# Optimization experiments

Measured on AMD Instinct MI355X. Metric: run time of the kernel, lower is better.

## Reference

```python
import jax, jax.numpy as jnp
import numpy as np

N, E, DIM, EDIM, H, T = 30000, 300000, 64, 16, 3, 6


def setup_inputs() -> dict:
    key = jax.random.key(0)
    ks = jax.random.split(key, 20)
    s = 0.1
    inp = {
        'x': jax.random.normal(ks[0], (N, DIM), jnp.float32),
        'edge_index': jax.random.randint(ks[1], (2, E), 0, N, jnp.int64),
        'edge_attr': jax.random.normal(ks[2], (E, EDIM), jnp.float32),
        # EdgeGATConv params (heads=3, out per head = DIM, concat=False -> head mean)
        'Wg': jax.random.normal(ks[3], (DIM, H * DIM), jnp.float32) * s,
        'bg': jnp.zeros((DIM,), jnp.float32),
        'a_src': jax.random.normal(ks[4], (H, DIM), jnp.float32) * s,
        'a_dst': jax.random.normal(ks[5], (H, DIM), jnp.float32) * s,
        'We': jax.random.normal(ks[6], (EDIM, H * DIM), jnp.float32) * s,
        'a_edge': jax.random.normal(ks[7], (H, DIM), jnp.float32) * s,
        # GRU (1 layer), torch gate order: r, z, n
        'Wih': jax.random.normal(ks[8], (3 * DIM, DIM), jnp.float32) * s,
        'Whh': jax.random.normal(ks[9], (3 * DIM, DIM), jnp.float32) * s,
        'bih': jnp.zeros((3 * DIM,), jnp.float32),
        'bhh': jnp.zeros((3 * DIM,), jnp.float32),
        # NodeLevelBatchNorm per time step
        'gamma': jnp.ones((T, DIM), jnp.float32),
        'beta': jnp.zeros((T, DIM), jnp.float32),
        # final linear: dim*(T+1) -> dim
        'Wlin': jax.random.normal(ks[10], (DIM * (T + 1), DIM), jnp.float32) * s,
        'blin': jnp.zeros((DIM,), jnp.float32),
    }
    return inp


def _edge_gat(x, edge_index, edge_attr, Wg, bg, a_src, a_dst, We, a_edge):
    n = x.shape[0]
    xw = (x @ Wg).reshape(n, H, DIM)                 # [N,H,C]
    ew = (edge_attr @ We).reshape(-1, H, DIM)        # [E,H,C]
    src, dst = edge_index[0], edge_index[1]
    logits = ((xw[src] * a_src).sum(-1)
              + (xw[dst] * a_dst).sum(-1)
              + (ew * a_edge).sum(-1))               # [E,H]
    logits = jax.nn.leaky_relu(logits, 0.2)
    # segment softmax over incoming edges per destination node
    amax = jax.ops.segment_max(logits, dst, num_segments=n)
    amax = jnp.where(jnp.isfinite(amax), amax, 0.0)
    ex = jnp.exp(logits - amax[dst])
    denom = jax.ops.segment_sum(ex, dst, num_segments=n)
    att = ex / (denom[dst] + 1e-16)                  # [E,H]
    agg = jax.ops.segment_sum(xw[src] * att[..., None], dst, num_segments=n)  # [N,H,C]
    return agg.mean(axis=1) + bg                     # concat=False: head mean


def _gru_step(m, h, Wih, Whh, bih, bhh):
    gi = m @ Wih.T + bih
    gh = h @ Whh.T + bhh
    ir, iz, inn = jnp.split(gi, 3, axis=-1)
    hr, hz, hn = jnp.split(gh, 3, axis=-1)
    r = jax.nn.sigmoid(ir + hr)
    z = jax.nn.sigmoid(iz + hz)
    nn_ = jnp.tanh(inn + r * hn)
    return (1.0 - z) * nn_ + z * h


def _node_bn(x, gamma, beta, eps=1e-5):
    mu = x.mean(axis=0)
    var = ((x - mu) ** 2).mean(axis=0)
    return (x - mu) * jax.lax.rsqrt(var + eps) * gamma + beta


def reference(x, edge_index, edge_attr, Wg, bg, a_src, a_dst, We, a_edge,
              Wih, Whh, bih, bhh, gamma, beta, Wlin, blin):
    h = x
    feats = [x]
    for i in range(T):
        m = jax.nn.celu(_edge_gat(x, edge_index, edge_attr, Wg, bg, a_src, a_dst, We, a_edge))
        h = _gru_step(m, h, Wih, Whh, bih, bhh)
        x = _node_bn(h, gamma[i], beta[i])
        feats.append(x)
    return jnp.concatenate(feats, axis=-1) @ Wlin + blin
```

## Files before the change

kernel.cpp:

```cpp
#include <hip/hip_runtime.h>
#include <math.h>

constexpr int N_ = 30000;
constexpr int E_ = 300000;
constexpr int SCB = (N_ + 255) / 256;

using f32x4  = __attribute__((ext_vector_type(4))) float;
using bf16x8 = __attribute__((ext_vector_type(8))) short;

__device__ __forceinline__ float4 ldg4(const float* p){ return *reinterpret_cast<const float4*>(p); }

__device__ __forceinline__ unsigned short f2bf(float f){
  union { float f; unsigned int u; } v; v.f = f;
  unsigned int r = v.u + 0x7FFFu + ((v.u >> 16) & 1u);
  return (unsigned short)(r >> 16);
}
__device__ __forceinline__ float bf2f(unsigned short b){
  union { unsigned int u; float f; } v; v.u = ((unsigned int)b) << 16;
  return v.f;
}
__device__ __forceinline__ float sigmoidf_(float x){ return 1.0f/(1.0f + __expf(-x)); }


__global__ void k_zero(int* __restrict__ deg){
  int i = blockIdx.x*256 + threadIdx.x;
  if (i < N_) deg[i] = 0;
}

__global__ void k_wfrag(const float* __restrict__ Wg, const float* __restrict__ Wih,
                        const float* __restrict__ Whh, const float* __restrict__ Wlin,
                        const float* __restrict__ We, const float* __restrict__ a_edge,
                        unsigned short* __restrict__ fG, unsigned short* __restrict__ fI,
                        unsigned short* __restrict__ fH, unsigned short* __restrict__ fL,
                        float* __restrict__ P){
  if (blockIdx.x == 256){
    int t = threadIdx.x; if (t >= 48) return;
    int j = t / 3, h = t % 3;
    float s = 0.f;
    for (int c = 0; c < 64; ++c) s += We[j*192 + h*64 + c] * a_edge[h*64 + c];
    P[j*3 + h] = s;
    return;
  }
  int id = blockIdx.x*256 + threadIdx.x;
  int lid, KT;
  unsigned short* dst; int mode;
  if (id < 12288)      { lid = id;         KT = 2;  dst = fG; mode = 0; }
  else if (id < 24576) { lid = id - 12288; KT = 2;  dst = fI; mode = 1; }
  else if (id < 36864) { lid = id - 24576; KT = 2;  dst = fH; mode = 2; }
  else                 { lid = id - 36864; KT = 14; dst = fL; mode = 3; }
  int j = lid & 7, l = (lid >> 3) & 63, rest = lid >> 9;
  int kt = rest % KT, nt = rest / KT;
  int k = kt*32 + (l>>4)*8 + j;
  int n = nt*16 + (l&15);
  float v;
  if (mode == 0)      v = Wg[k*192 + n];
  else if (mode == 1) v = Wih[n*64 + k];
  else if (mode == 2) v = Whh[n*64 + k];
  else                v = Wlin[k*64 + n];
  dst[lid] = f2bf(v);
}

__global__ void k_hist(const int* __restrict__ ei, int* __restrict__ deg){
  int e = blockIdx.x*256 + threadIdx.x;
  if (e < E_) atomicAdd(&deg[ei[E_ + e]], 1);
}

__global__ void k_scanA(const int* __restrict__ deg, int* __restrict__ partial){
  int i = blockIdx.x*256 + threadIdx.x;
  int v = (i < N_) ? deg[i] : 0;
  #pragma unroll
  for (int off = 1; off < 64; off <<= 1) v += __shfl_xor(v, off);
  __shared__ int ws[4];
  if ((threadIdx.x & 63) == 0) ws[threadIdx.x >> 6] = v;
  __syncthreads();
  if (threadIdx.x == 0) partial[blockIdx.x] = ws[0] + ws[1] + ws[2] + ws[3];
}

__global__ void k_scanB(int* __restrict__ partial, int* __restrict__ row_ptr){
  __shared__ int s[128];
  int t = threadIdx.x;
  int v = (t < SCB) ? partial[t] : 0;
  s[t] = v; __syncthreads();
  for (int off = 1; off < 128; off <<= 1){
    int u = (t >= off) ? s[t-off] : 0;
    __syncthreads();
    s[t] += u;
    __syncthreads();
  }
  if (t < SCB) partial[t] = s[t] - v;
  if (t == 0) row_ptr[N_] = E_;
}

__global__ void k_scanC(const int* __restrict__ deg, const int* __restrict__ partial,
                        int* __restrict__ row_ptr, int* __restrict__ cursor){
  __shared__ int s[256];
  int t = threadIdx.x, i = blockIdx.x*256 + t;
  int v = (i < N_) ? deg[i] : 0;
  s[t] = v; __syncthreads();
  for (int off = 1; off < 256; off <<= 1){
    int u = (t >= off) ? s[t-off] : 0;
    __syncthreads();
    s[t] += u;
    __syncthreads();
  }
  int ex = s[t] - v + partial[blockIdx.x];
  if (i < N_){ row_ptr[i] = ex; cursor[i] = ex; }
}

__global__ void k_scatter(const int* __restrict__ ei, const float* __restrict__ edge_attr,
                          const float* __restrict__ P,
                          int* __restrict__ cursor, int* __restrict__ src_s,
                          int* __restrict__ dst_s, float* __restrict__ el_s){
  __shared__ float sP[48];
  int t = threadIdx.x;
  if (t < 48) sP[t] = P[t];
  __syncthreads();
  int e = blockIdx.x*256 + t;
  if (e >= E_) return;
  const float* ea = edge_attr + (size_t)e*16;
  float v[16];
  #pragma unroll
  for (int q = 0; q < 4; ++q){
    float4 f = ldg4(ea + q*4);
    v[q*4+0]=f.x; v[q*4+1]=f.y; v[q*4+2]=f.z; v[q*4+3]=f.w;
  }
  float l0=0.f,l1=0.f,l2=0.f;
  #pragma unroll
  for (int j = 0; j < 16; ++j){
    l0 += v[j]*sP[j*3+0]; l1 += v[j]*sP[j*3+1]; l2 += v[j]*sP[j*3+2];
  }
  int d = ei[E_ + e];
  int p = atomicAdd(&cursor[d], 1);
  src_s[p] = ei[e];
  dst_s[p] = d;
  el_s[p*3+0] = l0; el_s[p*3+1] = l1; el_s[p*3+2] = l2;
}


__global__ __launch_bounds__(256) void k_xw(
    const float* __restrict__ hsrc,
    const float* __restrict__ bn_stats,
    const float* __restrict__ gamma, const float* __restrict__ beta,
    int gidx, int bn, int slot,
    const unsigned short* __restrict__ fG,
    const float* __restrict__ a_src, const float* __restrict__ a_dst,
    unsigned short* __restrict__ xw,
    float* __restrict__ asrc, float* __restrict__ adst,
    float* __restrict__ feats)
{
  __shared__ short sAf[8*64*8];
  __shared__ unsigned short sXW[64*196];
  __shared__ float sSc[64], sSh[64];
  const int t = threadIdx.x;
  const int row0 = blockIdx.x * 64;
  if (t < 64){
    float sc = 1.f, sh = 0.f;
    if (bn){
      float mu  = bn_stats[t] * (1.0f/30000.0f);
      float var = bn_stats[64+t] * (1.0f/30000.0f) - mu*mu;
      float rs = rsqrtf(var + 1e-5f);
      sc = gamma[gidx*64 + t] * rs;
      sh = beta[gidx*64 + t] - mu*sc;
    }
    sSc[t] = sc; sSh[t] = sh;
  }
  __syncthreads();
  {
    const int lr = t >> 4, k4 = (t & 15) * 4;
    const float sc0=sSc[k4],sc1=sSc[k4+1],sc2=sSc[k4+2],sc3=sSc[k4+3];
    const float sh0=sSh[k4],sh1=sSh[k4+1],sh2=sSh[k4+2],sh3=sSh[k4+3];
    const int kt = k4 >> 5, lanew = lr + (((k4>>3)&3)<<4), j0 = k4 & 7;
    #pragma unroll
    for (int i = 0; i < 4; ++i){
      int r = lr + i*16, gr = row0 + r;
      float4 v = make_float4(0.f,0.f,0.f,0.f);
      if (gr < N_){
        v = ldg4(hsrc + (size_t)gr*64 + k4);
        v.x = fmaf(v.x, sc0, sh0); v.y = fmaf(v.y, sc1, sh1);
        v.z = fmaf(v.z, sc2, sh2); v.w = fmaf(v.w, sc3, sh3);
        *reinterpret_cast<float4*>(feats + (size_t)gr*448 + slot*64 + k4) = v;
      }
      ushort4 pk; pk.x=f2bf(v.x); pk.y=f2bf(v.y); pk.z=f2bf(v.z); pk.w=f2bf(v.w);
      *reinterpret_cast<ushort4*>(&sAf[((i*2+kt)*64 + lanew)*8 + j0]) = pk;
    }
  }
  __syncthreads();
  const int w = t >> 6, l = t & 63, q = l >> 4, b = l & 15;
  f32x4 acc[12];
  #pragma unroll
  for (int nt = 0; nt < 12; ++nt) acc[nt] = (f32x4){0.f,0.f,0.f,0.f};
  bf16x8 a0 = *reinterpret_cast<bf16x8*>(&sAf[((w*2+0)*64 + l)*8]);
  bf16x8 a1 = *reinterpret_cast<bf16x8*>(&sAf[((w*2+1)*64 + l)*8]);
  #pragma unroll
  for (int nt = 0; nt < 12; ++nt){
    bf16x8 b0 = *reinterpret_cast<const bf16x8*>(fG + (size_t)((nt*2+0)*64 + l)*8);
    bf16x8 b1 = *reinterpret_cast<const bf16x8*>(fG + (size_t)((nt*2+1)*64 + l)*8);
    acc[nt] = __builtin_amdgcn_mfma_f32_16x16x32_bf16(a0, b0, acc[nt], 0, 0, 0);
    acc[nt] = __builtin_amdgcn_mfma_f32_16x16x32_bf16(a1, b1, acc[nt], 0, 0, 0);
  }
  float asl[3][4], adl[3][4];
  #pragma unroll
  for (int h = 0; h < 3; ++h)
    #pragma unroll
    for (int u = 0; u < 4; ++u){
      asl[h][u] = a_src[h*64 + u*16 + b];
      adl[h][u] = a_dst[h*64 + u*16 + b];
    }
  #pragma unroll
  for (int r = 0; r < 4; ++r){
    int gr = row0 + w*16 + q*4 + r;
    #pragma unroll
    for (int h = 0; h < 3; ++h){
      float s = 0.f, d = 0.f;
      #pragma unroll
      for (int u = 0; u < 4; ++u){
        s = fmaf(acc[4*h+u][r], asl[h][u], s);
        d = fmaf(acc[4*h+u][r], adl[h][u], d);
      }
      s += __shfl_xor(s,1); s += __shfl_xor(s,2); s += __shfl_xor(s,4); s += __shfl_xor(s,8);
      d += __shfl_xor(d,1); d += __shfl_xor(d,2); d += __shfl_xor(d,4); d += __shfl_xor(d,8);
      if (b == h && gr < N_){ asrc[gr*3+h] = s; adst[gr*3+h] = d; }
    }
  }
  #pragma unroll
  for (int nt = 0; nt < 12; ++nt){
    int col = nt*16 + b;
    #pragma unroll
    for (int r = 0; r < 4; ++r)
      sXW[(w*16 + q*4 + r)*196 + col] = f2bf(acc[nt][r]);
  }
  __syncthreads();
  #pragma unroll
  for (int i = 0; i < 12; ++i){
    int id = i*256 + t;
    int row = id / 48, cg = id % 48, gr = row0 + row;
    if (gr < N_){
      ushort4 pv = *reinterpret_cast<ushort4*>(&sXW[row*196 + cg*4]);
      *reinterpret_cast<ushort4*>(xw + (size_t)gr*192 + cg*4) = pv;
    }
  }
}

__global__ void k_att(const int* __restrict__ src_s, const int* __restrict__ dst_s,
                      const float* __restrict__ el_s,
                      const float* __restrict__ asrc, const float* __restrict__ adst,
                      float* __restrict__ att_s){
  int p = blockIdx.x*256 + threadIdx.x;
  if (p >= E_) return;
  int s = src_s[p], d = dst_s[p];
  #pragma unroll
  for (int h = 0; h < 3; ++h){
    float l = asrc[s*3+h] + adst[d*3+h] + el_s[p*3+h];
    l = l > 0.f ? l : 0.2f*l;
    att_s[p*3+h] = __expf(l);
  }
}

__global__ __launch_bounds__(256) void k_agg(
    const int* __restrict__ row_ptr, const int* __restrict__ src_s,
    const float* __restrict__ att_s,
    const unsigned short* __restrict__ xw,
    const float* __restrict__ bg,
    float* __restrict__ mbuf, float* __restrict__ bn_stats)
{
  if (blockIdx.x == 0 && threadIdx.x < 128) bn_stats[threadIdx.x] = 0.f;
  int n = blockIdx.x*4 + (threadIdx.x >> 6);
  int c = threadIdx.x & 63;
  if (n >= N_) return;
  int p0 = row_ptr[n], p1 = row_ptr[n+1];
  float d0 = 0.f, d1 = 0.f, d2 = 0.f;
  float a0 = 0.f, a1 = 0.f, a2 = 0.f;
  int p = p0;
  for (; p + 2 <= p1; p += 2){
    int sA = src_s[p], sB = src_s[p+1];
    float wA0 = att_s[p*3+0], wA1 = att_s[p*3+1], wA2 = att_s[p*3+2];
    float wB0 = att_s[p*3+3], wB1 = att_s[p*3+4], wB2 = att_s[p*3+5];
    const unsigned short* xpA = xw + (size_t)sA*192 + c;
    const unsigned short* xpB = xw + (size_t)sB*192 + c;
    float vA0 = bf2f(xpA[0]), vA1 = bf2f(xpA[64]), vA2 = bf2f(xpA[128]);
    float vB0 = bf2f(xpB[0]), vB1 = bf2f(xpB[64]), vB2 = bf2f(xpB[128]);
    d0 += wA0 + wB0; d1 += wA1 + wB1; d2 += wA2 + wB2;
    a0 = fmaf(wA0, vA0, a0); a1 = fmaf(wA1, vA1, a1); a2 = fmaf(wA2, vA2, a2);
    a0 = fmaf(wB0, vB0, a0); a1 = fmaf(wB1, vB1, a1); a2 = fmaf(wB2, vB2, a2);
  }
  if (p < p1){
    int s = src_s[p];
    float w0 = att_s[p*3+0], w1 = att_s[p*3+1], w2 = att_s[p*3+2];
    const unsigned short* xp = xw + (size_t)s*192 + c;
    d0 += w0; d1 += w1; d2 += w2;
    a0 = fmaf(w0, bf2f(xp[0]), a0);
    a1 = fmaf(w1, bf2f(xp[64]), a1);
    a2 = fmaf(w2, bf2f(xp[128]), a2);
  }
  float mp = (a0/(d0+1e-16f) + a1/(d1+1e-16f) + a2/(d2+1e-16f)) * (1.0f/3.0f) + bg[c];
  mbuf[(size_t)n*64 + c] = mp > 0.f ? mp : (__expf(mp) - 1.0f);
}

__global__ __launch_bounds__(256) void k_gru(
    const float* __restrict__ mbuf, const float* __restrict__ hsrc,
    float* __restrict__ hbuf,
    const unsigned short* __restrict__ fI, const unsigned short* __restrict__ fH,
    const float* __restrict__ bih, const float* __restrict__ bhh,
    float* __restrict__ bn_stats)
{
  __shared__ short sMf[8*64*8];
  __shared__ short sHf[8*64*8];
  __shared__ float sH[64][68];
  __shared__ float sStat[128];
  const int t = threadIdx.x;
  const int row0 = blockIdx.x * 64;
  if (t < 128) sStat[t] = 0.f;
  {
    const int lr = t >> 4, k4 = (t & 15) * 4;
    const int kt = k4 >> 5, lanew = lr + (((k4>>3)&3)<<4), j0 = k4 & 7;
    #pragma unroll
    for (int i = 0; i < 4; ++i){
      int r = lr + i*16, gr = row0 + r;
      float4 vm = make_float4(0.f,0.f,0.f,0.f), vh = vm;
      if (gr < N_){ vm = ldg4(mbuf + (size_t)gr*64 + k4); vh = ldg4(hsrc + (size_t)gr*64 + k4); }
      ushort4 pm; pm.x=f2bf(vm.x); pm.y=f2bf(vm.y); pm.z=f2bf(vm.z); pm.w=f2bf(vm.w);
      ushort4 ph; ph.x=f2bf(vh.x); ph.y=f2bf(vh.y); ph.z=f2bf(vh.z); ph.w=f2bf(vh.w);
      *reinterpret_cast<ushort4*>(&sMf[((i*2+kt)*64 + lanew)*8 + j0]) = pm;
      *reinterpret_cast<ushort4*>(&sHf[((i*2+kt)*64 + lanew)*8 + j0]) = ph;
      sH[r][k4+0]=vh.x; sH[r][k4+1]=vh.y; sH[r][k4+2]=vh.z; sH[r][k4+3]=vh.w;
    }
  }
  __syncthreads();
  const int w = t >> 6, l = t & 63, q = l >> 4, b = l & 15;
  f32x4 aI[12], aH[12];
  #pragma unroll
  for (int nt = 0; nt < 12; ++nt){ aI[nt] = (f32x4){0.f,0.f,0.f,0.f}; aH[nt] = (f32x4){0.f,0.f,0.f,0.f}; }
  bf16x8 am0 = *reinterpret_cast<bf16x8*>(&sMf[((w*2+0)*64 + l)*8]);
  bf16x8 am1 = *reinterpret_cast<bf16x8*>(&sMf[((w*2+1)*64 + l)*8]);
  bf16x8 ah0 = *reinterpret_cast<bf16x8*>(&sHf[((w*2+0)*64 + l)*8]);
  bf16x8 ah1 = *reinterpret_cast<bf16x8*>(&sHf[((w*2+1)*64 + l)*8]);
  #pragma unroll
  for (int nt = 0; nt < 12; ++nt){
    bf16x8 bI0 = *reinterpret_cast<const bf16x8*>(fI + (size_t)((nt*2+0)*64 + l)*8);
    bf16x8 bI1 = *reinterpret_cast<const bf16x8*>(fI + (size_t)((nt*2+1)*64 + l)*8);
    bf16x8 bH0 = *reinterpret_cast<const bf16x8*>(fH + (size_t)((nt*2+0)*64 + l)*8);
    bf16x8 bH1 = *reinterpret_cast<const bf16x8*>(fH + (size_t)((nt*2+1)*64 + l)*8);
    aI[nt] = __builtin_amdgcn_mfma_f32_16x16x32_bf16(am0, bI0, aI[nt], 0, 0, 0);
    aI[nt] = __builtin_amdgcn_mfma_f32_16x16x32_bf16(am1, bI1, aI[nt], 0, 0, 0);
    aH[nt] = __builtin_amdgcn_mfma_f32_16x16x32_bf16(ah0, bH0, aH[nt], 0, 0, 0);
    aH[nt] = __builtin_amdgcn_mfma_f32_16x16x32_bf16(ah1, bH1, aH[nt], 0, 0, 0);
  }
  float s1[4] = {0.f,0.f,0.f,0.f}, s2[4] = {0.f,0.f,0.f,0.f};
  #pragma unroll
  for (int tt = 0; tt < 4; ++tt){
    int c = tt*16 + b;
    float bir = bih[c], biz = bih[64+c], bin = bih[128+c];
    float bhr = bhh[c], bhz = bhh[64+c], bhn = bhh[128+c];
    #pragma unroll
    for (int r = 0; r < 4; ++r){
      int row = w*16 + q*4 + r, gr = row0 + row;
      float rg = sigmoidf_(aI[tt][r]   + bir + aH[tt][r]   + bhr);
      float zg = sigmoidf_(aI[tt+4][r] + biz + aH[tt+4][r] + bhz);
      float ng = tanhf(aI[tt+8][r] + bin + rg*(aH[tt+8][r] + bhn));
      float ho = sH[row][c];
      float hv = (1.f - zg)*ng + zg*ho;
      if (gr < N_){
        hbuf[(size_t)gr*64 + c] = hv;
        s1[tt] += hv; s2[tt] += hv*hv;
      }
    }
  }
  #pragma unroll
  for (int tt = 0; tt < 4; ++tt){
    float v = s1[tt];
    v += __shfl_xor(v, 16); v += __shfl_xor(v, 32);
    float u = s2[tt];
    u += __shfl_xor(u, 16); u += __shfl_xor(u, 32);
    if (q == 0){
      atomicAdd(&sStat[tt*16 + b], v);
      atomicAdd(&sStat[64 + tt*16 + b], u);
    }
  }
  __syncthreads();
  if (t < 128) atomicAdd(&bn_stats[t], sStat[t]);
}

__global__ __launch_bounds__(256) void k_final(
    const float* __restrict__ feats, const float* __restrict__ hbuf,
    const float* __restrict__ bn_stats,
    const float* __restrict__ gamma, const float* __restrict__ beta,
    const unsigned short* __restrict__ fL, const float* __restrict__ blin,
    float* __restrict__ out)
{
  __shared__ short sAf[8*64*8];
  __shared__ float sSc[64], sSh[64];
  const int t = threadIdx.x;
  const int row0 = blockIdx.x * 64;
  if (t < 64){
    float mu  = bn_stats[t] * (1.0f/30000.0f);
    float var = bn_stats[64+t] * (1.0f/30000.0f) - mu*mu;
    float rs = rsqrtf(var + 1e-5f);
    float sc = gamma[5*64 + t] * rs;
    sSc[t] = sc;
    sSh[t] = beta[5*64 + t] - mu*sc;
  }
  const int w = t >> 6, l = t & 63, q = l >> 4, b = l & 15;
  const int lr = t >> 4, k4 = (t & 15) * 4;
  const int kt = k4 >> 5, lanew = lr + (((k4>>3)&3)<<4), j0 = k4 & 7;
  f32x4 acc[4];
  #pragma unroll
  for (int nt = 0; nt < 4; ++nt) acc[nt] = (f32x4){0.f,0.f,0.f,0.f};
  for (int kc = 0; kc < 7; ++kc){
    __syncthreads();
    {
      #pragma unroll
      for (int i = 0; i < 4; ++i){
        int r = lr + i*16, gr = row0 + r;
        float4 v = make_float4(0.f,0.f,0.f,0.f);
        if (gr < N_){
          if (kc < 6) v = ldg4(feats + (size_t)gr*448 + kc*64 + k4);
          else {
            v = ldg4(hbuf + (size_t)gr*64 + k4);
            v.x = fmaf(v.x, sSc[k4+0], sSh[k4+0]);
            v.y = fmaf(v.y, sSc[k4+1], sSh[k4+1]);
            v.z = fmaf(v.z, sSc[k4+2], sSh[k4+2]);
            v.w = fmaf(v.w, sSc[k4+3], sSh[k4+3]);
          }
        }
        ushort4 pk; pk.x=f2bf(v.x); pk.y=f2bf(v.y); pk.z=f2bf(v.z); pk.w=f2bf(v.w);
        *reinterpret_cast<ushort4*>(&sAf[((i*2+kt)*64 + lanew)*8 + j0]) = pk;
      }
    }
    __syncthreads();
    bf16x8 a0 = *reinterpret_cast<bf16x8*>(&sAf[((w*2+0)*64 + l)*8]);
    bf16x8 a1 = *reinterpret_cast<bf16x8*>(&sAf[((w*2+1)*64 + l)*8]);
    #pragma unroll
    for (int nt = 0; nt < 4; ++nt){
      bf16x8 b0 = *reinterpret_cast<const bf16x8*>(fL + (size_t)((nt*14 + kc*2+0)*64 + l)*8);
      bf16x8 b1 = *reinterpret_cast<const bf16x8*>(fL + (size_t)((nt*14 + kc*2+1)*64 + l)*8);
      acc[nt] = __builtin_amdgcn_mfma_f32_16x16x32_bf16(a0, b0, acc[nt], 0, 0, 0);
      acc[nt] = __builtin_amdgcn_mfma_f32_16x16x32_bf16(a1, b1, acc[nt], 0, 0, 0);
    }
  }
  #pragma unroll
  for (int nt = 0; nt < 4; ++nt){
    int col = nt*16 + b;
    float bl = blin[col];
    #pragma unroll
    for (int r = 0; r < 4; ++r){
      int gr = row0 + w*16 + q*4 + r;
      if (gr < N_) out[(size_t)gr*64 + col] = acc[nt][r] + bl;
    }
  }
}


extern "C" void kernel_launch(void* const* d_in, const int* in_sizes, int n_in,
                              void* d_out, int out_size, void* d_ws, size_t ws_size,
                              hipStream_t stream) {
  const float* x        = (const float*)d_in[0];
  const int*   ei       = (const int*)  d_in[1];
  const float* edge_attr= (const float*)d_in[2];
  const float* Wg       = (const float*)d_in[3];
  const float* bg       = (const float*)d_in[4];
  const float* a_src    = (const float*)d_in[5];
  const float* a_dst    = (const float*)d_in[6];
  const float* We       = (const float*)d_in[7];
  const float* a_edge   = (const float*)d_in[8];
  const float* Wih      = (const float*)d_in[9];
  const float* Whh      = (const float*)d_in[10];
  const float* bih      = (const float*)d_in[11];
  const float* bhh      = (const float*)d_in[12];
  const float* gamma    = (const float*)d_in[13];
  const float* beta     = (const float*)d_in[14];
  const float* Wlin     = (const float*)d_in[15];
  const float* blin     = (const float*)d_in[16];
  float* out = (float*)d_out;

  char* w = (char*)d_ws;
  auto alloc = [&](size_t bytes) -> void* {
    void* p = (void*)w;
    w += (bytes + 255) & ~(size_t)255;
    return p;
  };
  int*   row_ptr = (int*)  alloc((size_t)(N_+1)*4);
  int*   deg     = (int*)  alloc((size_t)N_*4);
  int*   cursor  = (int*)  alloc((size_t)N_*4);
  int*   partial = (int*)  alloc(128*4);
  int*   src_s   = (int*)  alloc((size_t)E_*4);
  int*   dst_s   = (int*)  alloc((size_t)E_*4);
  float* el_s    = (float*)alloc((size_t)E_*3*4);
  float* att_s   = (float*)alloc((size_t)E_*3*4);
  float* Pw      = (float*)alloc(48*4);
  unsigned short* fG = (unsigned short*)alloc(12288*2);
  unsigned short* fI = (unsigned short*)alloc(12288*2);
  unsigned short* fH = (unsigned short*)alloc(12288*2);
  unsigned short* fL = (unsigned short*)alloc(28672*2);
  unsigned short* xw = (unsigned short*)alloc((size_t)N_*192*2);
  float* asrc    = (float*)alloc((size_t)N_*3*4);
  float* adst    = (float*)alloc((size_t)N_*3*4);
  float* mbuf    = (float*)alloc((size_t)N_*64*4);
  float* hbuf    = (float*)alloc((size_t)N_*64*4);
  float* feats   = (float*)alloc((size_t)N_*448*4);
  float* bn_stats= (float*)alloc(128*4);

  const int EB = (E_ + 255)/256;
  const int GEMMB = (N_ + 63)/64;

  k_zero   <<<SCB, 256, 0, stream>>>(deg);
  k_wfrag  <<<257, 256, 0, stream>>>(Wg, Wih, Whh, Wlin, We, a_edge, fG, fI, fH, fL, Pw);
  k_hist   <<<EB, 256, 0, stream>>>(ei, deg);
  k_scanA  <<<SCB, 256, 0, stream>>>(deg, partial);
  k_scanB  <<<1, 128, 0, stream>>>(partial, row_ptr);
  k_scanC  <<<SCB, 256, 0, stream>>>(deg, partial, row_ptr, cursor);
  k_scatter<<<EB, 256, 0, stream>>>(ei, edge_attr, Pw, cursor, src_s, dst_s, el_s);

  for (int step = 0; step < 6; ++step){
    const float* hsrc = (step == 0) ? x : hbuf;
    k_xw <<<GEMMB, 256, 0, stream>>>(hsrc, bn_stats, gamma, beta,
                                     step-1, step > 0 ? 1 : 0, step,
                                     fG, a_src, a_dst, xw, asrc, adst, feats);
    k_att<<<EB, 256, 0, stream>>>(src_s, dst_s, el_s, asrc, adst, att_s);
    k_agg<<<(N_+3)/4, 256, 0, stream>>>(row_ptr, src_s, att_s, xw, bg, mbuf, bn_stats);
    k_gru<<<GEMMB, 256, 0, stream>>>(mbuf, hsrc, hbuf, fI, fH, bih, bhh, bn_stats);
  }
  k_final<<<GEMMB, 256, 0, stream>>>(feats, hbuf, bn_stats, gamma, beta, fL, blin, out);
}
```

Before: 586.8 us.

## Store per-step features as bf16 MFMA fragments and interleave xw heads

Per-step normalized node features are no longer written as fp32 into a wide feats matrix. Instead k_xw dumps its bf16 A-fragments straight to a fragment buffer, and k_final reads them directly as MFMA operands without restaging through LDS. The xw layout is changed to an interleaved [node][channel][4] bf16 format so k_agg gathers all three heads with one 8-byte load per edge, and its edge loop is unrolled by 4. The deg zeroing kernel is folded into k_wfrag to save a launch. The cost is a padded xw (256 vs 192 entries per node) and a small extra fragment write per step.

```diff
diff --git a/kernel.cpp b/kernel.cpp
--- a/kernel.cpp
+++ b/kernel.cpp
@@ -4,6 +4,7 @@
 constexpr int N_ = 30000;
 constexpr int E_ = 300000;
 constexpr int SCB = (N_ + 255) / 256;
+constexpr int GB_ = (N_ + 63) / 64;
 
 using f32x4  = __attribute__((ext_vector_type(4))) float;
 using bf16x8 = __attribute__((ext_vector_type(8))) short;
@@ -21,18 +22,18 @@
 }
 __device__ __forceinline__ float sigmoidf_(float x){ return 1.0f/(1.0f + __expf(-x)); }
 
-
-__global__ void k_zero(int* __restrict__ deg){
-  int i = blockIdx.x*256 + threadIdx.x;
-  if (i < N_) deg[i] = 0;
-}
 
 __global__ void k_wfrag(const float* __restrict__ Wg, const float* __restrict__ Wih,
                         const float* __restrict__ Whh, const float* __restrict__ Wlin,
                         const float* __restrict__ We, const float* __restrict__ a_edge,
                         unsigned short* __restrict__ fG, unsigned short* __restrict__ fI,
                         unsigned short* __restrict__ fH, unsigned short* __restrict__ fL,
-                        float* __restrict__ P){
+                        float* __restrict__ P, int* __restrict__ deg){
+  if (blockIdx.x >= 257){
+    int i = (blockIdx.x - 257)*256 + threadIdx.x;
+    if (i < N_) deg[i] = 0;
+    return;
+  }
   if (blockIdx.x == 256){
     int t = threadIdx.x; if (t >= 48) return;
     int j = t / 3, h = t % 3;
@@ -141,12 +142,12 @@
     const float* __restrict__ hsrc,
     const float* __restrict__ bn_stats,
     const float* __restrict__ gamma, const float* __restrict__ beta,
-    int gidx, int bn, int slot,
+    int gidx, int bn,
     const unsigned short* __restrict__ fG,
     const float* __restrict__ a_src, const float* __restrict__ a_dst,
     unsigned short* __restrict__ xw,
     float* __restrict__ asrc, float* __restrict__ adst,
-    float* __restrict__ feats)
+    unsigned short* __restrict__ fr)
 {
   __shared__ short sAf[8*64*8];
   __shared__ unsigned short sXW[64*196];
@@ -178,13 +179,18 @@
         v = ldg4(hsrc + (size_t)gr*64 + k4);
         v.x = fmaf(v.x, sc0, sh0); v.y = fmaf(v.y, sc1, sh1);
         v.z = fmaf(v.z, sc2, sh2); v.w = fmaf(v.w, sc3, sh3);
-        *reinterpret_cast<float4*>(feats + (size_t)gr*448 + slot*64 + k4) = v;
       }
       ushort4 pk; pk.x=f2bf(v.x); pk.y=f2bf(v.y); pk.z=f2bf(v.z); pk.w=f2bf(v.w);
       *reinterpret_cast<ushort4*>(&sAf[((i*2+kt)*64 + lanew)*8 + j0]) = pk;
     }
   }
   __syncthreads();
+  {
+    bf16x8 v0 = *reinterpret_cast<bf16x8*>(&sAf[t*8]);
+    bf16x8 v1 = *reinterpret_cast<bf16x8*>(&sAf[2048 + t*8]);
+    bf16x8* g = reinterpret_cast<bf16x8*>(fr + (size_t)blockIdx.x*4096);
+    g[t] = v0; g[256 + t] = v1;
+  }
   const int w = t >> 6, l = t & 63, q = l >> 4, b = l & 15;
   f32x4 acc[12];
   #pragma unroll
@@ -231,12 +237,16 @@
   }
   __syncthreads();
   #pragma unroll
-  for (int i = 0; i < 12; ++i){
+  for (int i = 0; i < 16; ++i){
     int id = i*256 + t;
-    int row = id / 48, cg = id % 48, gr = row0 + row;
+    int row = id >> 6, c2 = id & 63, gr = row0 + row;
     if (gr < N_){
-      ushort4 pv = *reinterpret_cast<ushort4*>(&sXW[row*196 + cg*4]);
-      *reinterpret_cast<ushort4*>(xw + (size_t)gr*192 + cg*4) = pv;
+      ushort4 pv;
+      pv.x = sXW[row*196 + c2];
+      pv.y = sXW[row*196 + 64 + c2];
+      pv.z = sXW[row*196 + 128 + c2];
+      pv.w = 0;
+      *reinterpret_cast<ushort4*>(xw + ((size_t)gr << 8) + (c2 << 2)) = pv;
     }
   }
 }
@@ -271,26 +281,32 @@
   float d0 = 0.f, d1 = 0.f, d2 = 0.f;
   float a0 = 0.f, a1 = 0.f, a2 = 0.f;
   int p = p0;
-  for (; p + 2 <= p1; p += 2){
-    int sA = src_s[p], sB = src_s[p+1];
-    float wA0 = att_s[p*3+0], wA1 = att_s[p*3+1], wA2 = att_s[p*3+2];
-    float wB0 = att_s[p*3+3], wB1 = att_s[p*3+4], wB2 = att_s[p*3+5];
-    const unsigned short* xpA = xw + (size_t)sA*192 + c;
-    const unsigned short* xpB = xw + (size_t)sB*192 + c;
-    float vA0 = bf2f(xpA[0]), vA1 = bf2f(xpA[64]), vA2 = bf2f(xpA[128]);
-    float vB0 = bf2f(xpB[0]), vB1 = bf2f(xpB[64]), vB2 = bf2f(xpB[128]);
-    d0 += wA0 + wB0; d1 += wA1 + wB1; d2 += wA2 + wB2;
-    a0 = fmaf(wA0, vA0, a0); a1 = fmaf(wA1, vA1, a1); a2 = fmaf(wA2, vA2, a2);
-    a0 = fmaf(wB0, vB0, a0); a1 = fmaf(wB1, vB1, a1); a2 = fmaf(wB2, vB2, a2);
-  }
-  if (p < p1){
+  for (; p + 4 <= p1; p += 4){
+    int sA = src_s[p], sB = src_s[p+1], sC = src_s[p+2], sD = src_s[p+3];
+    ushort4 gA = *reinterpret_cast<const ushort4*>(xw + ((size_t)sA << 8) + (c << 2));
+    ushort4 gB = *reinterpret_cast<const ushort4*>(xw + ((size_t)sB << 8) + (c << 2));
+    ushort4 gC = *reinterpret_cast<const ushort4*>(xw + ((size_t)sC << 8) + (c << 2));
+    ushort4 gD = *reinterpret_cast<const ushort4*>(xw + ((size_t)sD << 8) + (c << 2));
+    float wA0 = att_s[p*3+0],  wA1 = att_s[p*3+1],  wA2 = att_s[p*3+2];
+    float wB0 = att_s[p*3+3],  wB1 = att_s[p*3+4],  wB2 = att_s[p*3+5];
+    float wC0 = att_s[p*3+6],  wC1 = att_s[p*3+7],  wC2 = att_s[p*3+8];
+    float wD0 = att_s[p*3+9],  wD1 = att_s[p*3+10], wD2 = att_s[p*3+11];
+    d0 += (wA0 + wB0) + (wC0 + wD0);
+    d1 += (wA1 + wB1) + (wC1 + wD1);
+    d2 += (wA2 + wB2) + (wC2 + wD2);
+    a0 = fmaf(wA0, bf2f(gA.x), a0); a1 = fmaf(wA1, bf2f(gA.y), a1); a2 = fmaf(wA2, bf2f(gA.z), a2);
+    a0 = fmaf(wB0, bf2f(gB.x), a0); a1 = fmaf(wB1, bf2f(gB.y), a1); a2 = fmaf(wB2, bf2f(gB.z), a2);
+    a0 = fmaf(wC0, bf2f(gC.x), a0); a1 = fmaf(wC1, bf2f(gC.y), a1); a2 = fmaf(wC2, bf2f(gC.z), a2);
+    a0 = fmaf(wD0, bf2f(gD.x), a0); a1 = fmaf(wD1, bf2f(gD.y), a1); a2 = fmaf(wD2, bf2f(gD.z), a2);
+  }
+  for (; p < p1; ++p){
     int s = src_s[p];
+    ushort4 g = *reinterpret_cast<const ushort4*>(xw + ((size_t)s << 8) + (c << 2));
     float w0 = att_s[p*3+0], w1 = att_s[p*3+1], w2 = att_s[p*3+2];
-    const unsigned short* xp = xw + (size_t)s*192 + c;
     d0 += w0; d1 += w1; d2 += w2;
-    a0 = fmaf(w0, bf2f(xp[0]), a0);
-    a1 = fmaf(w1, bf2f(xp[64]), a1);
-    a2 = fmaf(w2, bf2f(xp[128]), a2);
+    a0 = fmaf(w0, bf2f(g.x), a0);
+    a1 = fmaf(w1, bf2f(g.y), a1);
+    a2 = fmaf(w2, bf2f(g.z), a2);
   }
   float mp = (a0/(d0+1e-16f) + a1/(d1+1e-16f) + a2/(d2+1e-16f)) * (1.0f/3.0f) + bg[c];
   mbuf[(size_t)n*64 + c] = mp > 0.f ? mp : (__expf(mp) - 1.0f);
@@ -381,7 +397,7 @@
 }
 
 __global__ __launch_bounds__(256) void k_final(
-    const float* __restrict__ feats, const float* __restrict__ hbuf,
+    const unsigned short* __restrict__ ff, const float* __restrict__ hbuf,
     const float* __restrict__ bn_stats,
     const float* __restrict__ gamma, const float* __restrict__ beta,
     const unsigned short* __restrict__ fL, const float* __restrict__ blin,
@@ -399,40 +415,51 @@
     sSc[t] = sc;
     sSh[t] = beta[5*64 + t] - mu*sc;
   }
+  __syncthreads();
   const int w = t >> 6, l = t & 63, q = l >> 4, b = l & 15;
   const int lr = t >> 4, k4 = (t & 15) * 4;
   const int kt = k4 >> 5, lanew = lr + (((k4>>3)&3)<<4), j0 = k4 & 7;
+  {
+    #pragma unroll
+    for (int i = 0; i < 4; ++i){
+      int r = lr + i*16, gr = row0 + r;
+      float4 v = make_float4(0.f,0.f,0.f,0.f);
+      if (gr < N_){
+        v = ldg4(hbuf + (size_t)gr*64 + k4);
+        v.x = fmaf(v.x, sSc[k4+0], sSh[k4+0]);
+        v.y = fmaf(v.y, sSc[k4+1], sSh[k4+1]);
+        v.z = fmaf(v.z, sSc[k4+2], sSh[k4+2]);
+        v.w = fmaf(v.w, sSc[k4+3], sSh[k4+3]);
+      }
+      ushort4 pk; pk.x=f2bf(v.x); pk.y=f2bf(v.y); pk.z=f2bf(v.z); pk.w=f2bf(v.w);
+      *reinterpret_cast<ushort4*>(&sAf[((i*2+kt)*64 + lanew)*8 + j0]) = pk;
+    }
+  }
+  __syncthreads();
   f32x4 acc[4];
   #pragma unroll
   for (int nt = 0; nt < 4; ++nt) acc[nt] = (f32x4){0.f,0.f,0.f,0.f};
-  for (int kc = 0; kc < 7; ++kc){
-    __syncthreads();
-    {
-      #pragma unroll
-      for (int i = 0; i < 4; ++i){
-        int r = lr + i*16, gr = row0 + r;
-        float4 v = make_float4(0.f,0.f,0.f,0.f);
-        if (gr < N_){
-          if (kc < 6) v = ldg4(feats + (size_t)gr*448 + kc*64 + k4);
-          else {
-            v = ldg4(hbuf + (size_t)gr*64 + k4);
-            v.x = fmaf(v.x, sSc[k4+0], sSh[k4+0]);
-            v.y = fmaf(v.y, sSc[k4+1], sSh[k4+1]);
-            v.z = fmaf(v.z, sSc[k4+2], sSh[k4+2]);
-            v.w = fmaf(v.w, sSc[k4+3], sSh[k4+3]);
-          }
-        }
-        ushort4 pk; pk.x=f2bf(v.x); pk.y=f2bf(v.y); pk.z=f2bf(v.z); pk.w=f2bf(v.w);
-        *reinterpret_cast<ushort4*>(&sAf[((i*2+kt)*64 + lanew)*8 + j0]) = pk;
-      }
-    }
-    __syncthreads();
-    bf16x8 a0 = *reinterpret_cast<bf16x8*>(&sAf[((w*2+0)*64 + l)*8]);
-    bf16x8 a1 = *reinterpret_cast<bf16x8*>(&sAf[((w*2+1)*64 + l)*8]);
+  const unsigned short* fb = ff + (size_t)blockIdx.x*4096;
+  #pragma unroll
+  for (int kc = 0; kc < 6; ++kc){
+    const unsigned short* fs = fb + (size_t)kc*GB_*4096;
+    bf16x8 a0 = *reinterpret_cast<const bf16x8*>(fs + (w*2+0)*512 + l*8);
+    bf16x8 a1 = *reinterpret_cast<const bf16x8*>(fs + (w*2+1)*512 + l*8);
     #pragma unroll
     for (int nt = 0; nt < 4; ++nt){
       bf16x8 b0 = *reinterpret_cast<const bf16x8*>(fL + (size_t)((nt*14 + kc*2+0)*64 + l)*8);
       bf16x8 b1 = *reinterpret_cast<const bf16x8*>(fL + (size_t)((nt*14 + kc*2+1)*64 + l)*8);
+      acc[nt] = __builtin_amdgcn_mfma_f32_16x16x32_bf16(a0, b0, acc[nt], 0, 0, 0);
+      acc[nt] = __builtin_amdgcn_mfma_f32_16x16x32_bf16(a1, b1, acc[nt], 0, 0, 0);
+    }
+  }
+  {
+    bf16x8 a0 = *reinterpret_cast<bf16x8*>(&sAf[((w*2+0)*64 + l)*8]);
+    bf16x8 a1 = *reinterpret_cast<bf16x8*>(&sAf[((w*2+1)*64 + l)*8]);
+    #pragma unroll
+    for (int nt = 0; nt < 4; ++nt){
+      bf16x8 b0 = *reinterpret_cast<const bf16x8*>(fL + (size_t)((nt*14 + 12)*64 + l)*8);
+      bf16x8 b1 = *reinterpret_cast<const bf16x8*>(fL + (size_t)((nt*14 + 13)*64 + l)*8);
       acc[nt] = __builtin_amdgcn_mfma_f32_16x16x32_bf16(a0, b0, acc[nt], 0, 0, 0);
       acc[nt] = __builtin_amdgcn_mfma_f32_16x16x32_bf16(a1, b1, acc[nt], 0, 0, 0);
     }
@@ -491,19 +518,18 @@
   unsigned short* fI = (unsigned short*)alloc(12288*2);
   unsigned short* fH = (unsigned short*)alloc(12288*2);
   unsigned short* fL = (unsigned short*)alloc(28672*2);
-  unsigned short* xw = (unsigned short*)alloc((size_t)N_*192*2);
+  unsigned short* xw = (unsigned short*)alloc((size_t)N_*256*2);
+  unsigned short* ffrag = (unsigned short*)alloc((size_t)6*GB_*4096*2);
   float* asrc    = (float*)alloc((size_t)N_*3*4);
   float* adst    = (float*)alloc((size_t)N_*3*4);
   float* mbuf    = (float*)alloc((size_t)N_*64*4);
   float* hbuf    = (float*)alloc((size_t)N_*64*4);
-  float* feats   = (float*)alloc((size_t)N_*448*4);
   float* bn_stats= (float*)alloc(128*4);
 
   const int EB = (E_ + 255)/256;
-  const int GEMMB = (N_ + 63)/64;
-
-  k_zero   <<<SCB, 256, 0, stream>>>(deg);
-  k_wfrag  <<<257, 256, 0, stream>>>(Wg, Wih, Whh, Wlin, We, a_edge, fG, fI, fH, fL, Pw);
+
+  k_wfrag  <<<257 + SCB, 256, 0, stream>>>(Wg, Wih, Whh, Wlin, We, a_edge,
+                                           fG, fI, fH, fL, Pw, deg);
   k_hist   <<<EB, 256, 0, stream>>>(ei, deg);
   k_scanA  <<<SCB, 256, 0, stream>>>(deg, partial);
   k_scanB  <<<1, 128, 0, stream>>>(partial, row_ptr);
@@ -512,12 +538,13 @@
 
   for (int step = 0; step < 6; ++step){
     const float* hsrc = (step == 0) ? x : hbuf;
-    k_xw <<<GEMMB, 256, 0, stream>>>(hsrc, bn_stats, gamma, beta,
-                                     step-1, step > 0 ? 1 : 0, step,
-                                     fG, a_src, a_dst, xw, asrc, adst, feats);
+    k_xw <<<GB_, 256, 0, stream>>>(hsrc, bn_stats, gamma, beta,
+                                   step-1, step > 0 ? 1 : 0,
+                                   fG, a_src, a_dst, xw, asrc, adst,
+                                   ffrag + (size_t)step*GB_*4096);
     k_att<<<EB, 256, 0, stream>>>(src_s, dst_s, el_s, asrc, adst, att_s);
     k_agg<<<(N_+3)/4, 256, 0, stream>>>(row_ptr, src_s, att_s, xw, bg, mbuf, bn_stats);
-    k_gru<<<GEMMB, 256, 0, stream>>>(mbuf, hsrc, hbuf, fI, fH, bih, bhh, bn_stats);
-  }
-  k_final<<<GEMMB, 256, 0, stream>>>(feats, hbuf, bn_stats, gamma, beta, fL, blin, out);
-}
+    k_gru<<<GB_, 256, 0, stream>>>(mbuf, hsrc, hbuf, fI, fH, bih, bhh, bn_stats);
+  }
+  k_final<<<GB_, 256, 0, stream>>>(ffrag, hbuf, bn_stats, gamma, beta, fL, blin, out);
+}
```

Measured after the change: 559.0 us. 4.7% less time.
